# Kernel optimization log

Measured on AMD Instinct MI355X. Metric: run time of the kernel, lower is better.

Reference implementation:

```python
import jax, jax.numpy as jnp
import numpy as np

N, D, Q, V = 16384, 128, 16384, 64

def setup_inputs() -> dict:
    key = jax.random.key(0)
    k1, k2, k3 = jax.random.split(key, 3)
    points = jax.random.normal(k1, (N, D), dtype=jnp.float32)
    values = jax.random.normal(k2, (N, V), dtype=jnp.float32)
    points_q = jax.random.normal(k3, (Q, D), dtype=jnp.float32)
    return {"points": points, "values": values, "points_q": points_q}

def reference(points, values, points_q):
    # Squared Euclidean distances via GEMM form: |q|^2 - 2 q.p + |p|^2  -> [Q, N]
    q_sq = jnp.sum(points_q * points_q, axis=-1, keepdims=True)          # [Q, 1]
    p_sq = jnp.sum(points * points, axis=-1)                             # [N]
    dist2 = q_sq - 2.0 * jnp.einsum('qd,nd->qn', points_q, points) + p_sq
    nn_idx = jnp.argmin(dist2, axis=-1)                                  # [Q]
    return values[nn_idx]                                                # [Q, V]
```

## Files before the change

kernel.cpp:

```cpp
#include <hip/hip_runtime.h>

#define N_PTS 16384
#define DIMS  128
#define NQ    16384
#define NV    64
#define KT2   256
#define BK    64
#define BM    128
#define BN    128
#define CHUNK_NT 16
#define CHUNK_N  (BN * CHUNK_NT)
#define NCHUNK   (N_PTS / CHUNK_N)

typedef __attribute__((ext_vector_type(8))) _Float16 half8;
typedef __attribute__((ext_vector_type(4))) _Float16 half4;
typedef __attribute__((ext_vector_type(4))) float    f32x4;

#define QBLOCKS (NQ * DIMS / 1024)
#define PBLOCKS (N_PTS * DIMS / 1024)
__global__ __launch_bounds__(256) void split_fused(const float* __restrict__ q,
                                                   const float* __restrict__ pts,
                                                   _Float16* __restrict__ Aq,
                                                   _Float16* __restrict__ Bp,
                                                   float* __restrict__ p_sq,
                                                   unsigned long long* __restrict__ keys) {
    int t = blockIdx.x * 256 + threadIdx.x;
    if (t < NQ) keys[t] = ~0ull;
    const float* src;
    _Float16* dst;
    int t2;
    bool is_p = blockIdx.x >= QBLOCKS;
    if (is_p) { t2 = t - QBLOCKS * 256; src = pts; dst = Bp; }
    else      { t2 = t;                 src = q;   dst = Aq; }
    int idx4 = t2 * 4;
    int r = idx4 >> 7, c = idx4 & 127;
    float4 x = *(const float4*)(src + idx4);
    float xs[4] = {x.x, x.y, x.z, x.w};
    half4 h1, h2;
    float s = 0.f;
#pragma unroll
    for (int j = 0; j < 4; ++j) {
        _Float16 a = (_Float16)xs[j];
        h1[j] = a;
        h2[j] = (_Float16)(xs[j] - (float)a);
        s += xs[j] * xs[j];
    }
    _Float16* o = dst + (size_t)r * KT2 + c;
    *(half4*)o = h1; *(half4*)(o + 128) = h2;
    if (is_p) {
#pragma unroll
        for (int off = 1; off < 32; off <<= 1) s += __shfl_xor(s, off, 64);
        if ((threadIdx.x & 31) == 0) p_sq[r] = s;
    }
}

__device__ __forceinline__ unsigned int f2sortable(float f) {
    unsigned int b = __float_as_uint(f);
    return (b & 0x80000000u) ? ~b : (b | 0x80000000u);
}

__device__ __forceinline__ void gload16(const _Float16* g, const _Float16* l) {
    __builtin_amdgcn_global_load_lds((const __attribute__((address_space(1))) void*)g,
                                     (__attribute__((address_space(3))) void*)l, 16, 0, 0);
}

__global__ __launch_bounds__(256, 2) void nn_mfma(const _Float16* __restrict__ A,
                                                  const _Float16* __restrict__ B,
                                                  const float* __restrict__ p_sq,
                                                  unsigned long long* __restrict__ keys) {
    __shared__ _Float16 Ah1[2][BM * BK];
    __shared__ _Float16 Bsl[2][BN * BK];

    const int bid   = blockIdx.x;
    const int mtile = bid >> 3;
    const int chunk = bid & 7;
    const int nbase = chunk * CHUNK_N;

    const int tid = threadIdx.x;
    const int w   = tid >> 6;
    const int l   = tid & 63;
    const int wq  = w >> 1;
    const int wp  = w & 1;
    const int q16 = l >> 4;
    const int c16 = l & 15;

    const int srow = l >> 3;
    const int gch  = (l & 7) ^ (srow & 7);

    const _Float16* __restrict__ pa = A + (size_t)mtile * BM * KT2;
    const _Float16* __restrict__ pb = B + (size_t)nbase * KT2;

    int alane[4], ldsoff[4];
#pragma unroll
    for (int i = 0; i < 4; ++i) {
        alane[i]  = (w * 32 + i * 8 + srow) * KT2 + gch * 8;
        ldsoff[i] = (w * 32 + i * 8) * BK;
    }

    auto stageTo = [&](const _Float16* gbase, _Float16* lbase) {
#pragma unroll
        for (int i = 0; i < 4; ++i)
            gload16(gbase + alane[i], lbase + ldsoff[i]);
    };

    stageTo(pa,      &Ah1[0][0]);
    stageTo(pa + 64, &Ah1[1][0]);
    stageTo(pb,      &Bsl[0][0]);

    half8 ah2[2][2][4];
#pragma unroll
    for (int s = 0; s < 2; ++s)
#pragma unroll
        for (int ks = 0; ks < 2; ++ks)
#pragma unroll
            for (int mi = 0; mi < 4; ++mi) {
                int row = wq * 64 + mi * 16 + c16;
                ah2[s][ks][mi] = *(const half8*)(pa + (size_t)row * KT2 + 128 + s * 64 + ks * 32 + q16 * 8);
            }

    float    best[4][4];
    unsigned bpak[4][2];
#pragma unroll
    for (int mi = 0; mi < 4; ++mi) {
        best[mi][0] = best[mi][1] = best[mi][2] = best[mi][3] = 3.4e38f;
        bpak[mi][0] = bpak[mi][1] = 0;
    }

    f32x4 acc[4][4] = {};

    auto phaseL = [&](const _Float16* ah, const _Float16* bs) {
#pragma unroll
        for (int ks = 0; ks < 2; ++ks) {
            int slot8 = ((ks * 4 + q16) ^ (c16 & 7)) * 8;
            half8 a[4], b[4];
#pragma unroll
            for (int ni = 0; ni < 4; ++ni)
                b[ni] = *(const half8*)(bs + (wp * 64 + ni * 16 + c16) * BK + slot8);
#pragma unroll
            for (int mi = 0; mi < 4; ++mi)
                a[mi] = *(const half8*)(ah + (wq * 64 + mi * 16 + c16) * BK + slot8);
#pragma unroll
            for (int mi = 0; mi < 4; ++mi)
#pragma unroll
                for (int ni = 0; ni < 4; ++ni)
                    acc[mi][ni] = __builtin_amdgcn_mfma_f32_16x16x32_f16(a[mi], b[ni], acc[mi][ni], 0, 0, 0);
        }
    };
    auto phaseR = [&](int s, const _Float16* bs) {
#pragma unroll
        for (int ks = 0; ks < 2; ++ks) {
            int slot8 = ((ks * 4 + q16) ^ (c16 & 7)) * 8;
            half8 b[4];
#pragma unroll
            for (int ni = 0; ni < 4; ++ni)
                b[ni] = *(const half8*)(bs + (wp * 64 + ni * 16 + c16) * BK + slot8);
#pragma unroll
            for (int mi = 0; mi < 4; ++mi)
#pragma unroll
                for (int ni = 0; ni < 4; ++ni)
                    acc[mi][ni] = __builtin_amdgcn_mfma_f32_16x16x32_f16(ah2[s][ks][mi], b[ni], acc[mi][ni], 0, 0, 0);
        }
    };

#pragma unroll 1
    for (int nt = 0; nt < CHUNK_NT; ++nt) {
        const _Float16* pbn = pb + (size_t)nt * BN * KT2;

        float psq[4];
#pragma unroll
        for (int ni = 0; ni < 4; ++ni)
            psq[ni] = p_sq[nbase + nt * BN + wp * 64 + ni * 16 + c16];

        __syncthreads();
        phaseL(&Ah1[0][0], &Bsl[0][0]);

        __syncthreads();
        stageTo(pbn + 64, &Bsl[1][0]);
        phaseR(0, &Bsl[0][0]);

        __syncthreads();
        phaseL(&Ah1[1][0], &Bsl[1][0]);

        __syncthreads();
        stageTo(pbn + 128, &Bsl[0][0]);
        phaseR(1, &Bsl[1][0]);

        __syncthreads();
        stageTo(pbn + 192, &Bsl[1][0]);
        phaseL(&Ah1[0][0], &Bsl[0][0]);

        __syncthreads();
        if (nt + 1 < CHUNK_NT) stageTo(pbn + BN * KT2, &Bsl[0][0]);
        phaseL(&Ah1[1][0], &Bsl[1][0]);

#pragma unroll
        for (int mi = 0; mi < 4; ++mi)
#pragma unroll
            for (int reg = 0; reg < 4; ++reg) {
                float s0 = psq[0] - 2.0f * acc[mi][0][reg];
                float s1 = psq[1] - 2.0f * acc[mi][1][reg];
                float s2 = psq[2] - 2.0f * acc[mi][2][reg];
                float s3 = psq[3] - 2.0f * acc[mi][3][reg];
                float bv = s0; int bn2 = 0;
                if (s1 < bv) { bv = s1; bn2 = 1; }
                if (s2 < bv) { bv = s2; bn2 = 2; }
                if (s3 < bv) { bv = s3; bn2 = 3; }
                bool take = bv < best[mi][reg];
                unsigned lidx = (unsigned)(nt * BN + wp * 64 + (bn2 << 4) + c16);
                unsigned sh = (reg & 1) * 16;
                unsigned cur = bpak[mi][reg >> 1];
                unsigned nw  = (cur & ~(0xFFFFu << sh)) | (lidx << sh);
                best[mi][reg]      = take ? bv : best[mi][reg];
                bpak[mi][reg >> 1] = take ? nw : cur;
            }
#pragma unroll
        for (int mi = 0; mi < 4; ++mi)
#pragma unroll
            for (int ni = 0; ni < 4; ++ni)
                acc[mi][ni] = (f32x4)(0.f);
    }

#pragma unroll
    for (int mi = 0; mi < 4; ++mi)
#pragma unroll
        for (int reg = 0; reg < 4; ++reg) {
            float    bv   = best[mi][reg];
            unsigned lidx = (bpak[mi][reg >> 1] >> ((reg & 1) * 16)) & 0xFFFFu;
#pragma unroll
            for (int off = 1; off < 16; off <<= 1) {
                float    ov = __shfl_xor(bv, off, 64);
                unsigned oi = __shfl_xor((int)lidx, off, 64);
                if (ov < bv || (ov == bv && oi < lidx)) { bv = ov; lidx = oi; }
            }
            if (c16 == 0) {
                int row = mtile * BM + wq * 64 + mi * 16 + q16 * 4 + reg;
                unsigned long long key =
                    ((unsigned long long)f2sortable(bv) << 32) | (unsigned)(nbase + lidx);
                atomicMin(&keys[row], key);
            }
        }
}

__global__ __launch_bounds__(256) void gather_kernel(const unsigned long long* __restrict__ keys,
                                                     const float* __restrict__ values,
                                                     float* __restrict__ out) {
    int tid = threadIdx.x;
    int q = blockIdx.x * 16 + (tid >> 4);
    int c = tid & 15;
    int idx = (int)(keys[q] & 0xFFFFFFFFull);
    const float4* src = (const float4*)(values + (size_t)idx * NV);
    float4*       dst = (float4*)(out + (size_t)q * NV);
    dst[c] = src[c];
}

#define QT 64
#define PT 64
#define LSTRIDE 132
__global__ __launch_bounds__(256, 2) void nn_kernel(const float* __restrict__ points,
                                                    const float* __restrict__ values,
                                                    const float* __restrict__ pointsq,
                                                    const float* __restrict__ p_sq,
                                                    float* __restrict__ out) {
    __shared__ float lq[QT * LSTRIDE];
    __shared__ float lp[PT * LSTRIDE];
    __shared__ float lps[PT];
    __shared__ float red_val[QT][16];
    __shared__ int   red_idx[QT][16];
    __shared__ int   nn_idx[QT];

    const int tid = threadIdx.x;
    const int tx = tid & 15, ty = tid >> 4;
    const int qbase = blockIdx.x * QT;
    {
        int ql = tid >> 2, quad = tid & 3;
        const float4* src = (const float4*)(pointsq + (size_t)(qbase + ql) * DIMS);
#pragma unroll
        for (int j = 0; j < 8; ++j)
            *(float4*)(lq + ql * LSTRIDE + (quad + 4 * j) * 4) = src[quad + 4 * j];
    }
    float minv[4]; int mini[4];
#pragma unroll
    for (int qi = 0; qi < 4; ++qi) { minv[qi] = 3.4e38f; mini[qi] = 0; }
    for (int tile = 0; tile < N_PTS / PT; ++tile) {
        __syncthreads();
        {
            int pl = tid >> 2, quad = tid & 3;
            const float4* src = (const float4*)(points + (size_t)(tile * PT + pl) * DIMS);
#pragma unroll
            for (int j = 0; j < 8; ++j)
                *(float4*)(lp + pl * LSTRIDE + (quad + 4 * j) * 4) = src[quad + 4 * j];
            if (tid < PT) lps[tid] = p_sq[tile * PT + tid];
        }
        __syncthreads();
        float accl[4][4];
#pragma unroll
        for (int qi = 0; qi < 4; ++qi)
#pragma unroll
            for (int pi = 0; pi < 4; ++pi) accl[qi][pi] = 0.f;
        for (int kc = 0; kc < DIMS / 4; ++kc) {
            float4 aq[4], ap[4];
#pragma unroll
            for (int qi = 0; qi < 4; ++qi) aq[qi] = *(const float4*)(lq + (ty + 16 * qi) * LSTRIDE + kc * 4);
#pragma unroll
            for (int pi = 0; pi < 4; ++pi) ap[pi] = *(const float4*)(lp + (tx + 16 * pi) * LSTRIDE + kc * 4);
#pragma unroll
            for (int qi = 0; qi < 4; ++qi)
#pragma unroll
                for (int pi = 0; pi < 4; ++pi) {
                    accl[qi][pi] += aq[qi].x * ap[pi].x; accl[qi][pi] += aq[qi].y * ap[pi].y;
                    accl[qi][pi] += aq[qi].z * ap[pi].z; accl[qi][pi] += aq[qi].w * ap[pi].w;
                }
        }
#pragma unroll
        for (int qi = 0; qi < 4; ++qi)
#pragma unroll
            for (int pi = 0; pi < 4; ++pi) {
                float score = lps[tx + 16 * pi] - 2.f * accl[qi][pi];
                int idx = tile * PT + tx + 16 * pi;
                if (score < minv[qi]) { minv[qi] = score; mini[qi] = idx; }
            }
    }
    __syncthreads();
#pragma unroll
    for (int qi = 0; qi < 4; ++qi) { red_val[ty + 16 * qi][tx] = minv[qi]; red_idx[ty + 16 * qi][tx] = mini[qi]; }
    __syncthreads();
    if (tid < QT) {
        float bv = red_val[tid][0]; int bi = red_idx[tid][0];
#pragma unroll
        for (int t = 1; t < 16; ++t) {
            float v = red_val[tid][t]; int i = red_idx[tid][t];
            if (v < bv || (v == bv && i < bi)) { bv = v; bi = i; }
        }
        nn_idx[tid] = bi;
    }
    __syncthreads();
    {
        int ql = tid >> 2, quad = tid & 3;
        const float4* src = (const float4*)(values + (size_t)nn_idx[ql] * NV);
        float4* dst = (float4*)(out + (size_t)(qbase + ql) * NV);
#pragma unroll
        for (int j = 0; j < 4; ++j) dst[quad * 4 + j] = src[quad * 4 + j];
    }
}

__global__ __launch_bounds__(256) void psq_kernel(const float* __restrict__ points,
                                                  float* __restrict__ p_sq) {
    int row  = blockIdx.x * 4 + (threadIdx.x >> 6);
    int lane = threadIdx.x & 63;
    float2 v = *(const float2*)(points + row * DIMS + lane * 2);
    float s = v.x * v.x + v.y * v.y;
#pragma unroll
    for (int off = 32; off > 0; off >>= 1) s += __shfl_xor(s, off, 64);
    if (lane == 0) p_sq[row] = s;
}

extern "C" void kernel_launch(void* const* d_in, const int* in_sizes, int n_in,
                              void* d_out, int out_size, void* d_ws, size_t ws_size,
                              hipStream_t stream) {
    const float* points  = (const float*)d_in[0];
    const float* values  = (const float*)d_in[1];
    const float* pointsq = (const float*)d_in[2];
    float*       out     = (float*)d_out;

    const size_t OFF_KEYS = 0;
    const size_t OFF_PSQ  = 131072;
    const size_t OFF_A    = 196608;
    const size_t OFF_B    = OFF_A + (size_t)NQ * KT2 * 2;
    const size_t NEEDED   = OFF_B + (size_t)N_PTS * KT2 * 2;

    if (ws_size >= NEEDED) {
        unsigned long long* keys = (unsigned long long*)((char*)d_ws + OFF_KEYS);
        float*    p_sq = (float*)((char*)d_ws + OFF_PSQ);
        _Float16* Aq   = (_Float16*)((char*)d_ws + OFF_A);
        _Float16* Bp   = (_Float16*)((char*)d_ws + OFF_B);

        split_fused<<<QBLOCKS + PBLOCKS, 256, 0, stream>>>(pointsq, points, Aq, Bp, p_sq, keys);
        nn_mfma<<<(NQ / BM) * NCHUNK, 256, 0, stream>>>(Aq, Bp, p_sq, keys);
        gather_kernel<<<NQ / 16, 256, 0, stream>>>(keys, values, out);
    } else {
        float* p_sq = (float*)d_ws;
        psq_kernel<<<N_PTS / 4, 256, 0, stream>>>(points, p_sq);
        nn_kernel<<<NQ / QT, 256, 0, stream>>>(points, values, pointsq, p_sq, out);
    }
}
```

Measured before the change: 263.8 us.

## Keep all A fragments in registers and restage B with fewer barriers

All four 64-wide K slices of the query tile are now loaded into registers once, so A no longer goes through LDS and the per-step A fragment reads are gone. LDS is reused as a deeper B buffer: each B slab feeds two MFMA slices in a row, and each N-tile needs three barriers instead of six. The cost is many more VGPRs for the A fragments (32 half8 per lane), which can cause spills or lower occupancy under the launch bound of 2 blocks.

```diff
diff --git a/kernel.cpp b/kernel.cpp
--- a/kernel.cpp
+++ b/kernel.cpp
@@ -68,8 +68,7 @@
                                                   const _Float16* __restrict__ B,
                                                   const float* __restrict__ p_sq,
                                                   unsigned long long* __restrict__ keys) {
-    __shared__ _Float16 Ah1[2][BM * BK];
-    __shared__ _Float16 Bsl[2][BN * BK];
+    __shared__ _Float16 Bs[2][2][BN * BK];
 
     const int bid   = blockIdx.x;
     const int mtile = bid >> 3;
@@ -90,32 +89,30 @@
     const _Float16* __restrict__ pa = A + (size_t)mtile * BM * KT2;
     const _Float16* __restrict__ pb = B + (size_t)nbase * KT2;
 
-    int alane[4], ldsoff[4];
+    int blane[4], ldsoff[4];
 #pragma unroll
     for (int i = 0; i < 4; ++i) {
-        alane[i]  = (w * 32 + i * 8 + srow) * KT2 + gch * 8;
+        blane[i]  = (w * 32 + i * 8 + srow) * KT2 + gch * 8;
         ldsoff[i] = (w * 32 + i * 8) * BK;
     }
 
     auto stageTo = [&](const _Float16* gbase, _Float16* lbase) {
 #pragma unroll
         for (int i = 0; i < 4; ++i)
-            gload16(gbase + alane[i], lbase + ldsoff[i]);
+            gload16(gbase + blane[i], lbase + ldsoff[i]);
     };
 
-    stageTo(pa,      &Ah1[0][0]);
-    stageTo(pa + 64, &Ah1[1][0]);
-    stageTo(pb,      &Bsl[0][0]);
-
-    half8 ah2[2][2][4];
-#pragma unroll
-    for (int s = 0; s < 2; ++s)
+    stageTo(pb, &Bs[0][0][0]);
+
+    half8 af[4][2][4];
+#pragma unroll
+    for (int s = 0; s < 4; ++s)
 #pragma unroll
         for (int ks = 0; ks < 2; ++ks)
 #pragma unroll
             for (int mi = 0; mi < 4; ++mi) {
                 int row = wq * 64 + mi * 16 + c16;
-                ah2[s][ks][mi] = *(const half8*)(pa + (size_t)row * KT2 + 128 + s * 64 + ks * 32 + q16 * 8);
+                af[s][ks][mi] = *(const half8*)(pa + (size_t)row * KT2 + s * 64 + ks * 32 + q16 * 8);
             }
 
     float    best[4][4];
@@ -128,25 +125,7 @@
 
     f32x4 acc[4][4] = {};
 
-    auto phaseL = [&](const _Float16* ah, const _Float16* bs) {
-#pragma unroll
-        for (int ks = 0; ks < 2; ++ks) {
-            int slot8 = ((ks * 4 + q16) ^ (c16 & 7)) * 8;
-            half8 a[4], b[4];
-#pragma unroll
-            for (int ni = 0; ni < 4; ++ni)
-                b[ni] = *(const half8*)(bs + (wp * 64 + ni * 16 + c16) * BK + slot8);
-#pragma unroll
-            for (int mi = 0; mi < 4; ++mi)
-                a[mi] = *(const half8*)(ah + (wq * 64 + mi * 16 + c16) * BK + slot8);
-#pragma unroll
-            for (int mi = 0; mi < 4; ++mi)
-#pragma unroll
-                for (int ni = 0; ni < 4; ++ni)
-                    acc[mi][ni] = __builtin_amdgcn_mfma_f32_16x16x32_f16(a[mi], b[ni], acc[mi][ni], 0, 0, 0);
-        }
-    };
-    auto phaseR = [&](int s, const _Float16* bs) {
+    auto segDual = [&](const _Float16* bs, const half8 (&a0)[2][4], const half8 (&a1)[2][4]) {
 #pragma unroll
         for (int ks = 0; ks < 2; ++ks) {
             int slot8 = ((ks * 4 + q16) ^ (c16 & 7)) * 8;
@@ -158,13 +137,34 @@
             for (int mi = 0; mi < 4; ++mi)
 #pragma unroll
                 for (int ni = 0; ni < 4; ++ni)
-                    acc[mi][ni] = __builtin_amdgcn_mfma_f32_16x16x32_f16(ah2[s][ks][mi], b[ni], acc[mi][ni], 0, 0, 0);
+                    acc[mi][ni] = __builtin_amdgcn_mfma_f32_16x16x32_f16(a0[ks][mi], b[ni], acc[mi][ni], 0, 0, 0);
+#pragma unroll
+            for (int mi = 0; mi < 4; ++mi)
+#pragma unroll
+                for (int ni = 0; ni < 4; ++ni)
+                    acc[mi][ni] = __builtin_amdgcn_mfma_f32_16x16x32_f16(a1[ks][mi], b[ni], acc[mi][ni], 0, 0, 0);
+        }
+    };
+    auto segOne = [&](const _Float16* bs, const half8 (&a0)[2][4]) {
+#pragma unroll
+        for (int ks = 0; ks < 2; ++ks) {
+            int slot8 = ((ks * 4 + q16) ^ (c16 & 7)) * 8;
+            half8 b[4];
+#pragma unroll
+            for (int ni = 0; ni < 4; ++ni)
+                b[ni] = *(const half8*)(bs + (wp * 64 + ni * 16 + c16) * BK + slot8);
+#pragma unroll
+            for (int mi = 0; mi < 4; ++mi)
+#pragma unroll
+                for (int ni = 0; ni < 4; ++ni)
+                    acc[mi][ni] = __builtin_amdgcn_mfma_f32_16x16x32_f16(a0[ks][mi], b[ni], acc[mi][ni], 0, 0, 0);
         }
     };
 
 #pragma unroll 1
     for (int nt = 0; nt < CHUNK_NT; ++nt) {
         const _Float16* pbn = pb + (size_t)nt * BN * KT2;
+        const int h0 = (nt * 3) & 1;
 
         float psq[4];
 #pragma unroll
@@ -172,26 +172,19 @@
             psq[ni] = p_sq[nbase + nt * BN + wp * 64 + ni * 16 + c16];
 
         __syncthreads();
-        phaseL(&Ah1[0][0], &Bsl[0][0]);
-
-        __syncthreads();
-        stageTo(pbn + 64, &Bsl[1][0]);
-        phaseR(0, &Bsl[0][0]);
-
-        __syncthreads();
-        phaseL(&Ah1[1][0], &Bsl[1][0]);
-
-        __syncthreads();
-        stageTo(pbn + 128, &Bsl[0][0]);
-        phaseR(1, &Bsl[1][0]);
-
-        __syncthreads();
-        stageTo(pbn + 192, &Bsl[1][0]);
-        phaseL(&Ah1[0][0], &Bsl[0][0]);
-
-        __syncthreads();
-        if (nt + 1 < CHUNK_NT) stageTo(pbn + BN * KT2, &Bsl[0][0]);
-        phaseL(&Ah1[1][0], &Bsl[1][0]);
+        stageTo(pbn + 64, &Bs[h0 ^ 1][0][0]);
+        segDual(&Bs[h0][0][0], af[0], af[2]);
+
+        __syncthreads();
+        stageTo(pbn + 128, &Bs[h0][0][0]);
+        stageTo(pbn + 192, &Bs[h0][1][0]);
+        segDual(&Bs[h0 ^ 1][0][0], af[1], af[3]);
+
+        __syncthreads();
+        if (nt + 1 < CHUNK_NT)
+            stageTo(pbn + BN * KT2, &Bs[h0 ^ 1][0][0]);
+        segOne(&Bs[h0][0][0], af[0]);
+        segOne(&Bs[h0][1][0], af[1]);
 
 #pragma unroll
         for (int mi = 0; mi < 4; ++mi)
```

After: 390.9 us. 48.2% more time.

## Triple-buffer B tiles and merge split-K phases to halve barriers

Applied to the files above, without the earlier changes.

Grows the B staging buffer in shared memory from two slots to three and rotates them across N-tiles. Each B segment is now consumed by both A halves in one merged pass, so the per-tile schedule drops from six barriers to three. Async global-to-LDS loads are issued earlier, giving each B segment more lead time before it is used. The cost is 16 KB more shared memory per block, which could limit occupancy at two blocks per CU, and more register pressure from the larger fused MFMA segments.

```diff
diff --git a/kernel.cpp b/kernel.cpp
--- a/kernel.cpp
+++ b/kernel.cpp
@@ -69,7 +69,7 @@
                                                   const float* __restrict__ p_sq,
                                                   unsigned long long* __restrict__ keys) {
     __shared__ _Float16 Ah1[2][BM * BK];
-    __shared__ _Float16 Bsl[2][BN * BK];
+    __shared__ _Float16 Bsl[3][BN * BK];
 
     const int bid   = blockIdx.x;
     const int mtile = bid >> 3;
@@ -90,17 +90,17 @@
     const _Float16* __restrict__ pa = A + (size_t)mtile * BM * KT2;
     const _Float16* __restrict__ pb = B + (size_t)nbase * KT2;
 
-    int alane[4], ldsoff[4];
+    int blane[4], ldsoff[4];
 #pragma unroll
     for (int i = 0; i < 4; ++i) {
-        alane[i]  = (w * 32 + i * 8 + srow) * KT2 + gch * 8;
+        blane[i]  = (w * 32 + i * 8 + srow) * KT2 + gch * 8;
         ldsoff[i] = (w * 32 + i * 8) * BK;
     }
 
     auto stageTo = [&](const _Float16* gbase, _Float16* lbase) {
 #pragma unroll
         for (int i = 0; i < 4; ++i)
-            gload16(gbase + alane[i], lbase + ldsoff[i]);
+            gload16(gbase + blane[i], lbase + ldsoff[i]);
     };
 
     stageTo(pa,      &Ah1[0][0]);
@@ -128,7 +128,7 @@
 
     f32x4 acc[4][4] = {};
 
-    auto phaseL = [&](const _Float16* ah, const _Float16* bs) {
+    auto segDual = [&](const _Float16* ah, const half8 (&ar)[2][4], const _Float16* bs) {
 #pragma unroll
         for (int ks = 0; ks < 2; ++ks) {
             int slot8 = ((ks * 4 + q16) ^ (c16 & 7)) * 8;
@@ -144,23 +144,35 @@
 #pragma unroll
                 for (int ni = 0; ni < 4; ++ni)
                     acc[mi][ni] = __builtin_amdgcn_mfma_f32_16x16x32_f16(a[mi], b[ni], acc[mi][ni], 0, 0, 0);
+#pragma unroll
+            for (int mi = 0; mi < 4; ++mi)
+#pragma unroll
+                for (int ni = 0; ni < 4; ++ni)
+                    acc[mi][ni] = __builtin_amdgcn_mfma_f32_16x16x32_f16(ar[ks][mi], b[ni], acc[mi][ni], 0, 0, 0);
         }
     };
-    auto phaseR = [&](int s, const _Float16* bs) {
+    auto segOne = [&](const _Float16* ah, const _Float16* bs) {
 #pragma unroll
         for (int ks = 0; ks < 2; ++ks) {
             int slot8 = ((ks * 4 + q16) ^ (c16 & 7)) * 8;
-            half8 b[4];
+            half8 a[4], b[4];
 #pragma unroll
             for (int ni = 0; ni < 4; ++ni)
                 b[ni] = *(const half8*)(bs + (wp * 64 + ni * 16 + c16) * BK + slot8);
 #pragma unroll
             for (int mi = 0; mi < 4; ++mi)
+                a[mi] = *(const half8*)(ah + (wq * 64 + mi * 16 + c16) * BK + slot8);
+#pragma unroll
+            for (int mi = 0; mi < 4; ++mi)
 #pragma unroll
                 for (int ni = 0; ni < 4; ++ni)
-                    acc[mi][ni] = __builtin_amdgcn_mfma_f32_16x16x32_f16(ah2[s][ks][mi], b[ni], acc[mi][ni], 0, 0, 0);
+                    acc[mi][ni] = __builtin_amdgcn_mfma_f32_16x16x32_f16(a[mi], b[ni], acc[mi][ni], 0, 0, 0);
         }
     };
+
+    _Float16* p0 = &Bsl[0][0];
+    _Float16* p1 = &Bsl[1][0];
+    _Float16* p2 = &Bsl[2][0];
 
 #pragma unroll 1
     for (int nt = 0; nt < CHUNK_NT; ++nt) {
@@ -172,26 +184,22 @@
             psq[ni] = p_sq[nbase + nt * BN + wp * 64 + ni * 16 + c16];
 
         __syncthreads();
-        phaseL(&Ah1[0][0], &Bsl[0][0]);
-
-        __syncthreads();
-        stageTo(pbn + 64, &Bsl[1][0]);
-        phaseR(0, &Bsl[0][0]);
-
-        __syncthreads();
-        phaseL(&Ah1[1][0], &Bsl[1][0]);
-
-        __syncthreads();
-        stageTo(pbn + 128, &Bsl[0][0]);
-        phaseR(1, &Bsl[1][0]);
-
-        __syncthreads();
-        stageTo(pbn + 192, &Bsl[1][0]);
-        phaseL(&Ah1[0][0], &Bsl[0][0]);
-
-        __syncthreads();
-        if (nt + 1 < CHUNK_NT) stageTo(pbn + BN * KT2, &Bsl[0][0]);
-        phaseL(&Ah1[1][0], &Bsl[1][0]);
+        stageTo(pbn + 64, p1);
+        segDual(&Ah1[0][0], ah2[0], p0);
+
+        __syncthreads();
+        stageTo(pbn + 128, p2);
+        stageTo(pbn + 192, p0);
+        segDual(&Ah1[1][0], ah2[1], p1);
+
+        __syncthreads();
+        if (nt + 1 < CHUNK_NT)
+            stageTo(pbn + BN * KT2, p1);
+        segOne(&Ah1[0][0], p2);
+        segOne(&Ah1[1][0], p0);
+
+        _Float16* t0 = p0;
+        p0 = p1; p1 = p2; p2 = t0;
 
 #pragma unroll
         for (int mi = 0; mi < 4; ++mi)
```

Result: faster. 256.6 us, median of 2 (-2.7%).
